# Kernel tuning notes

Measured on AMD Instinct MI355X. Metric: run time of the kernel, lower is better.

## Reference

```python
import jax, jax.numpy as jnp
import numpy as np

M, N, T = 32, 32, 512
H1 = (M + N) * 10 * 8      # 5120
H2 = M * N * 4             # 4096
HID = 1000                 # GRU hidden (hardcoded in module)
EPS = 1e-12


def _l2norm(x):
    # torch.nn.functional.normalize: x / max(||x||_2, eps)
    return x / jnp.maximum(jnp.linalg.norm(x), EPS)


def setup_inputs() -> dict:
    key = jax.random.key(0)
    ks = jax.random.split(key, 16)
    rn = lambda k, shp, s: (jax.random.normal(k, shp, dtype=jnp.float32) * s)
    inp = {
        "y": rn(ks[0], (T, N), 1.0),
        "F": rn(ks[1], (M, M), 0.5 / np.sqrt(M)),   # stable dynamics
        "H": rn(ks[2], (N, M), 1.0 / np.sqrt(M)),
        "m1x0": rn(ks[3], (M,), 1.0),
        "h0": rn(ks[4], (HID,), 1.0),
        "W1": rn(ks[5], (H1, M + N), 1.0 / np.sqrt(M + N)),
        "b1": rn(ks[6], (H1,), 0.01),
        "Wih": rn(ks[7], (3 * HID, H1), 1.0 / np.sqrt(H1)),
        "bih": rn(ks[8], (3 * HID,), 0.01),
        "Whh": rn(ks[9], (3 * HID, HID), 1.0 / np.sqrt(HID)),
        "bhh": rn(ks[10], (3 * HID,), 0.01),
        "W2": rn(ks[11], (H2, HID), 1.0 / np.sqrt(HID)),
        "b2": rn(ks[12], (H2,), 0.01),
        "W3": rn(ks[13], (M * N, H2), 1.0 / np.sqrt(H2)),
        "b3": rn(ks[14], (M * N,), 0.01),
    }
    return inp


def reference(y, F, H, m1x0, h0, W1, b1, Wih, bih, Whh, bhh, W2, b2, W3, b3):
    m, n = F.shape[0], H.shape[0]

    def step(carry, yt):
        m1x_prior, m1x_post, h = carry
        # step_prior
        m1x_prev_prior = m1x_prior
        m1x_prior = F @ m1x_post              # [m]
        m1y = H @ m1x_prior                   # [n]
        # step_KGain_est: features
        dm1x_n = _l2norm(m1x_post - m1x_prev_prior)
        dm1y_n = _l2norm(yt - m1y)
        kin = jnp.concatenate([dm1y_n, dm1x_n])  # [n+m]
        # KGain_step: Linear+ReLU -> single-step GRU -> Linear+ReLU -> Linear
        x = jax.nn.relu(W1 @ kin + b1)        # [H1]
        gi = Wih @ x + bih                    # [3*HID]
        gh = Whh @ h + bhh
        ir, iz, ic = jnp.split(gi, 3)
        hr, hz, hc = jnp.split(gh, 3)
        r = jax.nn.sigmoid(ir + hr)
        z = jax.nn.sigmoid(iz + hz)
        c = jnp.tanh(ic + r * hc)
        h_new = (1.0 - z) * c + z * h         # GRU hidden [HID]
        l2 = jax.nn.relu(W2 @ h_new + b2)     # [H2]
        KG = (W3 @ l2 + b3).reshape(m, n)     # Kalman gain
        # KNet_step: innovation update
        m1x_post_new = m1x_prior + KG @ (yt - m1y)
        return (m1x_prior, m1x_post_new, h_new), m1x_post_new

    init = (m1x0, m1x0, h0)
    _, posts = jax.lax.scan(step, init, y)
    return posts  # [T, m]
```

## Files before the change

kernel.cpp:

```cpp
#include <hip/hip_runtime.h>
#include <cmath>

#define Mdim 32
#define Ndim 32
#define Tsteps 512
#define H1dim 5120
#define H2dim 4096
#define HIDdim 1000
#define NWG 256
#define NTHR 1024

typedef unsigned int u32;
typedef unsigned short u16;

__device__ u16 g_w2b[H2dim * HIDdim];
__device__ u16 g_w3t[H2dim * Mdim * Ndim];

#define OFF_WIH 0
#define OFF_WHH 122880
#define OFF_UNION 146880
#define OFF_H9 157120
#define OFF_MISC 161640
#define SMEM_BYTES 162560

#define MI_POST 0
#define MI_PRIOR 32
#define MI_PREV 64
#define MI_INNOV 96
#define MI_KIN 128
#define MI_GI 192
#define MI_GH 204

__device__ __forceinline__ u16 f2bf(float f) {
  u32 u = __float_as_uint(f);
  return (u16)((u + 0x7fffu + ((u >> 16) & 1u)) >> 16);
}
__device__ __forceinline__ float bflo(u32 u) { return __uint_as_float(u << 16); }
__device__ __forceinline__ float bfhi(u32 u) { return __uint_as_float(u & 0xffff0000u); }

__device__ __forceinline__ float dot4(float4 a, float4 b) {
  return a.x * b.x + a.y * b.y + a.z * b.z + a.w * b.w;
}
__device__ __forceinline__ float dot8_bb(uint4 a, uint4 b) {
  float s = 0.f;
  s = fmaf(bflo(a.x), bflo(b.x), s); s = fmaf(bfhi(a.x), bfhi(b.x), s);
  s = fmaf(bflo(a.y), bflo(b.y), s); s = fmaf(bfhi(a.y), bfhi(b.y), s);
  s = fmaf(bflo(a.z), bflo(b.z), s); s = fmaf(bfhi(a.z), bfhi(b.z), s);
  s = fmaf(bflo(a.w), bflo(b.w), s); s = fmaf(bfhi(a.w), bfhi(b.w), s);
  return s;
}
__device__ __forceinline__ float dot8_bf(uint4 a, const float* x8) {
  float s = 0.f;
  s = fmaf(bflo(a.x), x8[0], s); s = fmaf(bfhi(a.x), x8[1], s);
  s = fmaf(bflo(a.y), x8[2], s); s = fmaf(bfhi(a.y), x8[3], s);
  s = fmaf(bflo(a.z), x8[4], s); s = fmaf(bfhi(a.z), x8[5], s);
  s = fmaf(bflo(a.w), x8[6], s); s = fmaf(bfhi(a.w), x8[7], s);
  return s;
}

__device__ __forceinline__ float wave_reduce64(float v) {
#pragma unroll
  for (int off = 32; off >= 1; off >>= 1) v += __shfl_xor(v, off, 64);
  return v;
}
__device__ __forceinline__ float group16_reduce(float v) {
#pragma unroll
  for (int off = 8; off >= 1; off >>= 1) v += __shfl_xor(v, off, 64);
  return v;
}

__device__ __forceinline__ float4 ldg_cg4(const float* p) {
  float4 r;
  asm volatile("global_load_dwordx4 %0, %1, off sc0 sc1\n\ts_waitcnt vmcnt(0)"
               : "=v"(r) : "v"(p) : "memory");
  return r;
}
__device__ __forceinline__ uint4 ldg_cg4u(const void* p) {
  uint4 r;
  asm volatile("global_load_dwordx4 %0, %1, off sc0 sc1\n\ts_waitcnt vmcnt(0)"
               : "=v"(r) : "v"(p) : "memory");
  return r;
}
__device__ __forceinline__ void ldg2_cg4(const float* p0, const float* p1,
                                         float4& r0, float4& r1) {
  asm volatile("global_load_dwordx4 %0, %2, off sc0 sc1\n\t"
               "global_load_dwordx4 %1, %3, off sc0 sc1\n\t"
               "s_waitcnt vmcnt(0)"
               : "=&v"(r0), "=&v"(r1) : "v"(p0), "v"(p1) : "memory");
}
__device__ __forceinline__ void stg_cg1(float* p, float v) {
  asm volatile("global_store_dword %0, %1, off sc0 sc1" :: "v"(p), "v"(v) : "memory");
}
__device__ __forceinline__ void stg_cg_u16(u16* p, u16 v) {
  u32 vv = v;
  asm volatile("global_store_short %0, %1, off sc0 sc1" :: "v"(p), "v"(vv) : "memory");
}

__device__ __forceinline__ void gridbar(u32* bar, u32 nb) {
  asm volatile("s_waitcnt vmcnt(0)" ::: "memory");
  __syncthreads();
  if (threadIdx.x == 0) {
    u32 g = (u32)blockIdx.x & 15u;
    u32 a = __hip_atomic_fetch_add(bar + g * 16, 1u, __ATOMIC_RELAXED,
                                   __HIP_MEMORY_SCOPE_AGENT);
    if ((a & 15u) == 15u) {
      u32 b = __hip_atomic_fetch_add(bar + 256, 1u, __ATOMIC_RELAXED,
                                     __HIP_MEMORY_SCOPE_AGENT);
      if ((b & 15u) == 15u)
        __hip_atomic_fetch_add(bar + 320, 1u, __ATOMIC_RELAXED,
                               __HIP_MEMORY_SCOPE_AGENT);
    }
    while (__hip_atomic_load(bar + 320, __ATOMIC_RELAXED,
                             __HIP_MEMORY_SCOPE_AGENT) < nb)
      __builtin_amdgcn_s_sleep(2);
  }
  __syncthreads();
}

__global__ void convert_w2(const float* __restrict__ W2) {
  int i = blockIdx.x * 1024 + threadIdx.x;
  if (i < H2dim * HIDdim) g_w2b[i] = f2bf(W2[i]);
}

__global__ void convert_w3t(const float* __restrict__ W3) {
  __shared__ float tile[32][33];
  int tr = blockIdx.x >> 7;
  int tc = blockIdx.x & 127;
  int r0 = tr * 32, c0 = tc * 32;
  int j = threadIdx.x & 31, i0 = threadIdx.x >> 5;
#pragma unroll
  for (int p = 0; p < 4; ++p) {
    int i = i0 + p * 8;
    tile[i][j] = W3[(size_t)(r0 + i) * H2dim + c0 + j];
  }
  __syncthreads();
#pragma unroll
  for (int p = 0; p < 4; ++p) {
    int i = i0 + p * 8;
    g_w3t[(size_t)(c0 + i) * 1024 + r0 + j] = f2bf(tile[j][i]);
  }
}

__global__ void __launch_bounds__(NTHR)
knet_kernel(const float* __restrict__ y, const float* __restrict__ F,
            const float* __restrict__ Hm, const float* __restrict__ m1x0,
            const float* __restrict__ h0, const float* __restrict__ W1,
            const float* __restrict__ b1, const float* __restrict__ Wih,
            const float* __restrict__ bih, const float* __restrict__ Whh,
            const float* __restrict__ bhh, const float* __restrict__ b2,
            const float* __restrict__ b3, float* __restrict__ out,
            u32* bar, u16* xb, float* hbuf, float* dpart) {
  extern __shared__ char smem[];
  u16* s_wih = (u16*)(smem + OFF_WIH);
  u16* s_whh = (u16*)(smem + OFF_WHH);
  u16* s_x = (u16*)(smem + OFF_UNION);
  float4* s_red4 = (float4*)(smem + OFF_UNION);
  float* s_redf = (float*)(smem + OFF_UNION);
  float* s_pd = (float*)(smem + OFF_UNION);
  float* s_h9 = (float*)(smem + OFF_H9);
  float* s_m = (float*)(smem + OFF_MISC);
  float* s_post = s_m + MI_POST;
  float* s_prior = s_m + MI_PRIOR;
  float* s_prev = s_m + MI_PREV;
  float* s_innov = s_m + MI_INNOV;
  float* s_kin = s_m + MI_KIN;
  float* s_gi = s_m + MI_GI;
  float* s_gh = s_m + MI_GH;

  const int tid = threadIdx.x;
  const int w = tid >> 6;
  const int lane = tid & 63;
  const int wg = blockIdx.x;
  const int k0 = wg * 4;
  const bool gru_wg = (wg < 250);
  u32 nb = 0;

  if (gru_wg) {
#pragma unroll 1
    for (int r = 0; r < 12; ++r) {
      const float* src = Wih + (size_t)((r >> 2) * HIDdim + k0 + (r & 3)) * H1dim;
      u16* dst = s_wih + r * H1dim;
      for (int e = tid; e < H1dim; e += NTHR) dst[e] = f2bf(src[e]);
    }
#pragma unroll 1
    for (int r = 0; r < 12; ++r) {
      const float* src = Whh + (size_t)((r >> 2) * HIDdim + k0 + (r & 3)) * HIDdim;
      u16* dst = s_whh + r * HIDdim;
      for (int e = tid; e < HIDdim; e += NTHR) dst[e] = f2bf(src[e]);
    }
  }
  if (tid < 250) {
    float4 hv = ((const float4*)h0)[tid];
    int b0 = tid * 4;
    s_h9[((b0 + 0) >> 3) * 9 + ((b0 + 0) & 7)] = hv.x;
    s_h9[((b0 + 1) >> 3) * 9 + ((b0 + 1) & 7)] = hv.y;
    s_h9[((b0 + 2) >> 3) * 9 + ((b0 + 2) & 7)] = hv.z;
    s_h9[((b0 + 3) >> 3) * 9 + ((b0 + 3) & 7)] = hv.w;
  }
  if (tid < Mdim) s_prior[tid] = m1x0[tid];
  __syncthreads();

  for (int t = 0; t < Tsteps; ++t) {
    if (t > 0) {
      float4 a0, a1;
      ldg2_cg4(dpart + tid * 4, dpart + (tid + 1024) * 4, a0, a1);
      float4 s;
      s.x = a0.x + a1.x; s.y = a0.y + a1.y; s.z = a0.z + a1.z; s.w = a0.w + a1.w;
#pragma unroll
      for (int off = 8; off <= 32; off <<= 1) {
        s.x += __shfl_xor(s.x, off, 64);
        s.y += __shfl_xor(s.y, off, 64);
        s.z += __shfl_xor(s.z, off, 64);
        s.w += __shfl_xor(s.w, off, 64);
      }
      if (lane < 8) s_red4[w * 8 + lane] = s;
    }
    __syncthreads();
    if (tid < Mdim) {
      float p;
      if (t == 0) {
        p = m1x0[tid];
      } else {
        float d = 0.f;
#pragma unroll
        for (int ww = 0; ww < 16; ++ww) d += s_redf[ww * 32 + tid];
        float bb = 0.f;
#pragma unroll 8
        for (int j = 0; j < 32; ++j) bb = fmaf(b3[tid * 32 + j], s_innov[j], bb);
        p = s_prior[tid] + d + bb;
        if (wg == 0) out[(t - 1) * Mdim + tid] = p;
      }
      s_prev[tid] = s_prior[tid];
      s_post[tid] = p;
    }
    __syncthreads();
    if (tid < Mdim) {
      float s = 0.f;
      const float4* Fr = (const float4*)(F + tid * Mdim);
      const float4* pp = (const float4*)s_post;
#pragma unroll
      for (int j = 0; j < 8; ++j) s += dot4(Fr[j], pp[j]);
      s_prior[tid] = s;
    }
    __syncthreads();
    if (tid < Ndim) {
      float s = 0.f;
      const float4* Hr = (const float4*)(Hm + tid * Mdim);
      const float4* pp = (const float4*)s_prior;
#pragma unroll
      for (int j = 0; j < 8; ++j) s += dot4(Hr[j], pp[j]);
      s_innov[tid] = y[t * Ndim + tid] - s;
    }
    __syncthreads();
    if (tid < 64) {
      float v = (tid < Ndim) ? s_innov[tid] : (s_post[tid - Ndim] - s_prev[tid - Ndim]);
      float sq = v * v;
#pragma unroll
      for (int off = 16; off >= 1; off >>= 1) sq += __shfl_xor(sq, off, 32);
      s_kin[tid] = v / fmaxf(sqrtf(sq), 1e-12f);
    }
    __syncthreads();
    if (w < 5) {
      int g = lane >> 4, k = lane & 15;
      int row = wg * 20 + w * 4 + g;
      float s = dot4(((const float4*)W1)[row * 16 + k], ((const float4*)s_kin)[k]);
      s = group16_reduce(s);
      if (k == 0) stg_cg_u16(xb + row, f2bf(fmaxf(s + b1[row], 0.f)));
    } else if (gru_wg && w >= 12) {
      int base = (w - 12) * 3;
#pragma unroll
      for (int rr = 0; rr < 3; ++rr) {
        int r = base + rr;
        const uint4* wr = (const uint4*)(s_whh + r * HIDdim);
        float acc = dot8_bf(wr[lane], s_h9 + lane * 9);
        if (lane < 61) acc += dot8_bf(wr[lane + 64], s_h9 + (lane + 64) * 9);
        acc = wave_reduce64(acc);
        if (lane == 0) s_gh[r] = acc + bhh[(r >> 2) * HIDdim + k0 + (r & 3)];
      }
    }
    gridbar(bar, ++nb);

    if (gru_wg) {
      if (tid < 640) ((uint4*)s_x)[tid] = ldg_cg4u((const char*)xb + tid * 16);
      __syncthreads();
      if (w < 12) {
        const uint4* wr = (const uint4*)(s_wih + w * H1dim);
        const uint4* xr = (const uint4*)s_x;
        float acc = 0.f;
#pragma unroll
        for (int i = 0; i < 10; ++i) {
          int j = lane + 64 * i;
          acc += dot8_bb(wr[j], xr[j]);
        }
        acc = wave_reduce64(acc);
        if (lane == 0) s_gi[w] = acc + bih[(w >> 2) * HIDdim + k0 + (w & 3)];
      }
      __syncthreads();
      if (tid < 4) {
        int k = k0 + tid;
        float hold = s_h9[(k >> 3) * 9 + (k & 7)];
        float ir = s_gi[tid], iz = s_gi[4 + tid], ic = s_gi[8 + tid];
        float r = 1.f / (1.f + expf(-(ir + s_gh[tid])));
        float z = 1.f / (1.f + expf(-(iz + s_gh[4 + tid])));
        float c_ = tanhf(ic + r * s_gh[8 + tid]);
        stg_cg1(hbuf + k, (1.f - z) * c_ + z * hold);
      }
    }
    gridbar(bar, ++nb);

    if (tid < 250) {
      float4 hv = ldg_cg4(hbuf + tid * 4);
      int b0 = tid * 4;
      s_h9[((b0 + 0) >> 3) * 9 + ((b0 + 0) & 7)] = hv.x;
      s_h9[((b0 + 1) >> 3) * 9 + ((b0 + 1) & 7)] = hv.y;
      s_h9[((b0 + 2) >> 3) * 9 + ((b0 + 2) & 7)] = hv.z;
      s_h9[((b0 + 3) >> 3) * 9 + ((b0 + 3) & 7)] = hv.w;
    }
    __syncthreads();
    {
      int c = wg * 16 + w;
      const uint4* wr = (const uint4*)(g_w2b + (size_t)c * HIDdim);
      float acc = dot8_bf(wr[lane], s_h9 + lane * 9);
      if (lane < 61) acc += dot8_bf(wr[lane + 64], s_h9 + (lane + 64) * 9);
      acc = wave_reduce64(acc);
      float l2c = fmaxf(acc + b2[c], 0.f);
      const uint4* tr3 = (const uint4*)(g_w3t + (size_t)c * 1024);
      uint4 t0 = tr3[2 * lane], t1 = tr3[2 * lane + 1];
      const float* iv = s_innov + 16 * (lane & 1);
      float u = dot8_bf(t0, iv) + dot8_bf(t1, iv + 8);
      u += __shfl_xor(u, 1, 64);
      if ((lane & 1) == 0) s_pd[w * 32 + (lane >> 1)] = l2c * u;
    }
    __syncthreads();
    if (tid < 32) {
      float pdv = 0.f;
#pragma unroll
      for (int ww = 0; ww < 16; ++ww) pdv += s_pd[ww * 32 + tid];
      stg_cg1(dpart + wg * 32 + tid, pdv);
    }
    gridbar(bar, ++nb);
  }

  if (wg == 0) {
    float4 a0, a1;
    ldg2_cg4(dpart + tid * 4, dpart + (tid + 1024) * 4, a0, a1);
    float4 s;
    s.x = a0.x + a1.x; s.y = a0.y + a1.y; s.z = a0.z + a1.z; s.w = a0.w + a1.w;
#pragma unroll
    for (int off = 8; off <= 32; off <<= 1) {
      s.x += __shfl_xor(s.x, off, 64);
      s.y += __shfl_xor(s.y, off, 64);
      s.z += __shfl_xor(s.z, off, 64);
      s.w += __shfl_xor(s.w, off, 64);
    }
    if (lane < 8) s_red4[w * 8 + lane] = s;
    __syncthreads();
    if (tid < Mdim) {
      float d = 0.f;
#pragma unroll
      for (int ww = 0; ww < 16; ++ww) d += s_redf[ww * 32 + tid];
      float bb = 0.f;
#pragma unroll 8
      for (int j = 0; j < 32; ++j) bb = fmaf(b3[tid * 32 + j], s_innov[j], bb);
      out[(Tsteps - 1) * Mdim + tid] = s_prior[tid] + d + bb;
    }
  }
}

extern "C" void kernel_launch(void* const* d_in, const int* in_sizes, int n_in,
                              void* d_out, int out_size, void* d_ws, size_t ws_size,
                              hipStream_t stream) {
  const float* y    = (const float*)d_in[0];
  const float* F    = (const float*)d_in[1];
  const float* Hm   = (const float*)d_in[2];
  const float* m1x0 = (const float*)d_in[3];
  const float* h0   = (const float*)d_in[4];
  const float* W1   = (const float*)d_in[5];
  const float* b1   = (const float*)d_in[6];
  const float* Wih  = (const float*)d_in[7];
  const float* bih  = (const float*)d_in[8];
  const float* Whh  = (const float*)d_in[9];
  const float* bhh  = (const float*)d_in[10];
  const float* W2   = (const float*)d_in[11];
  const float* b2   = (const float*)d_in[12];
  const float* W3   = (const float*)d_in[13];
  const float* b3   = (const float*)d_in[14];
  float* out = (float*)d_out;

  u32* bar   = (u32*)d_ws;
  u16* xb    = (u16*)((char*)d_ws + 4096);
  float* hbuf  = (float*)((char*)d_ws + 14336);
  float* dpart = (float*)((char*)d_ws + 18432);

  convert_w2<<<4000, 1024, 0, stream>>>(W2);
  convert_w3t<<<4096, 256, 0, stream>>>(W3);
  hipMemsetAsync(d_ws, 0, 4096, stream);
  hipFuncSetAttribute((const void*)knet_kernel,
                      hipFuncAttributeMaxDynamicSharedMemorySize, SMEM_BYTES);
  void* args[] = {&y, &F, &Hm, &m1x0, &h0, &W1, &b1, &Wih, &bih, &Whh, &bhh,
                  &b2, &b3, &out, &bar, &xb, &hbuf, &dpart};
  hipLaunchCooperativeKernel((const void*)knet_kernel, dim3(NWG), dim3(NTHR),
                             args, SMEM_BYTES, stream);
}
```

Measured before the change: 7.523 ms.

## Split grid barrier into arrive/wait and overlap independent work in the gaps

Replaces the hierarchical atomic grid barrier with a single-counter barrier split into arrive and wait phases. Work that does not depend on the barrier is moved between arrive and wait: the Whh·h product for the next step, the W3^T·innovation dot, the b3 term and the next y load. Per-block W2, W3, W1 and b2 weights are hoisted into registers once before the time loop. The small Kalman prior/innovation chain now runs inside one wave without block syncs. The aim is to shorten the serial per-step critical path dominated by grid barriers, but all 256 blocks now contend on a single atomic counter and register pressure rises.

```diff
diff --git a/kernel.cpp b/kernel.cpp
--- a/kernel.cpp
+++ b/kernel.cpp
@@ -9,6 +9,7 @@
 #define HIDdim 1000
 #define NWG 256
 #define NTHR 1024
+#define POLLER 320
 
 typedef unsigned int u32;
 typedef unsigned short u16;
@@ -25,7 +26,6 @@
 
 #define MI_POST 0
 #define MI_PRIOR 32
-#define MI_PREV 64
 #define MI_INNOV 96
 #define MI_KIN 128
 #define MI_GI 192
@@ -96,23 +96,16 @@
   asm volatile("global_store_short %0, %1, off sc0 sc1" :: "v"(p), "v"(vv) : "memory");
 }
 
-__device__ __forceinline__ void gridbar(u32* bar, u32 nb) {
+__device__ __forceinline__ void gb_arrive(u32* bar) {
   asm volatile("s_waitcnt vmcnt(0)" ::: "memory");
   __syncthreads();
-  if (threadIdx.x == 0) {
-    u32 g = (u32)blockIdx.x & 15u;
-    u32 a = __hip_atomic_fetch_add(bar + g * 16, 1u, __ATOMIC_RELAXED,
-                                   __HIP_MEMORY_SCOPE_AGENT);
-    if ((a & 15u) == 15u) {
-      u32 b = __hip_atomic_fetch_add(bar + 256, 1u, __ATOMIC_RELAXED,
-                                     __HIP_MEMORY_SCOPE_AGENT);
-      if ((b & 15u) == 15u)
-        __hip_atomic_fetch_add(bar + 320, 1u, __ATOMIC_RELAXED,
-                               __HIP_MEMORY_SCOPE_AGENT);
-    }
-    while (__hip_atomic_load(bar + 320, __ATOMIC_RELAXED,
-                             __HIP_MEMORY_SCOPE_AGENT) < nb)
-      __builtin_amdgcn_s_sleep(2);
+  if (threadIdx.x == POLLER)
+    __hip_atomic_fetch_add(bar, 1u, __ATOMIC_RELAXED, __HIP_MEMORY_SCOPE_AGENT);
+}
+__device__ __forceinline__ void gb_wait(u32* bar, u32 target) {
+  if (threadIdx.x == POLLER) {
+    while (__hip_atomic_load(bar, __ATOMIC_RELAXED, __HIP_MEMORY_SCOPE_AGENT) < target)
+      __builtin_amdgcn_s_sleep(1);
   }
   __syncthreads();
 }
@@ -161,7 +154,6 @@
   float* s_m = (float*)(smem + OFF_MISC);
   float* s_post = s_m + MI_POST;
   float* s_prior = s_m + MI_PRIOR;
-  float* s_prev = s_m + MI_PREV;
   float* s_innov = s_m + MI_INNOV;
   float* s_kin = s_m + MI_KIN;
   float* s_gi = s_m + MI_GI;
@@ -197,8 +189,44 @@
     s_h9[((b0 + 2) >> 3) * 9 + ((b0 + 2) & 7)] = hv.z;
     s_h9[((b0 + 3) >> 3) * 9 + ((b0 + 3) & 7)] = hv.w;
   }
-  if (tid < Mdim) s_prior[tid] = m1x0[tid];
   __syncthreads();
+
+  const int c2 = wg * 16 + w;
+  const uint4* w2p = (const uint4*)(g_w2b + (size_t)c2 * HIDdim);
+  uint4 wr0r = w2p[lane];
+  uint4 wr1r = make_uint4(0u, 0u, 0u, 0u);
+  if (lane < 61) wr1r = w2p[lane + 64];
+  const uint4* w3p = (const uint4*)(g_w3t + (size_t)c2 * 1024);
+  uint4 t0r = w3p[2 * lane];
+  uint4 t1r = w3p[2 * lane + 1];
+  const float b2c = b2[c2];
+  float4 w1c = make_float4(0.f, 0.f, 0.f, 0.f);
+  float b1c = 0.f;
+  int w1row = 0;
+  if (w < 5) {
+    w1row = wg * 20 + w * 4 + (lane >> 4);
+    w1c = ((const float4*)W1)[w1row * 16 + (lane & 15)];
+    b1c = b1[w1row];
+  }
+  float prior = 0.f, bb = 0.f, yv = 0.f;
+  if (w == 0 && lane < 32) {
+    prior = m1x0[lane];
+    yv = y[lane];
+  }
+
+  auto gh_compute = [&]() {
+    int base = (w - 12) * 3;
+#pragma unroll
+    for (int rr = 0; rr < 3; ++rr) {
+      int r = base + rr;
+      const uint4* wr = (const uint4*)(s_whh + r * HIDdim);
+      float acc = dot8_bf(wr[lane], s_h9 + lane * 9);
+      if (lane < 61) acc += dot8_bf(wr[lane + 64], s_h9 + (lane + 64) * 9);
+      acc = wave_reduce64(acc);
+      if (lane == 0) s_gh[r] = acc + bhh[(r >> 2) * HIDdim + k0 + (r & 3)];
+    }
+  };
+  if (gru_wg && w >= 12) gh_compute();
 
   for (int t = 0; t < Tsteps; ++t) {
     if (t > 0) {
@@ -216,69 +244,57 @@
       if (lane < 8) s_red4[w * 8 + lane] = s;
     }
     __syncthreads();
-    if (tid < Mdim) {
-      float p;
-      if (t == 0) {
-        p = m1x0[tid];
-      } else {
-        float d = 0.f;
-#pragma unroll
-        for (int ww = 0; ww < 16; ++ww) d += s_redf[ww * 32 + tid];
-        float bb = 0.f;
-#pragma unroll 8
-        for (int j = 0; j < 32; ++j) bb = fmaf(b3[tid * 32 + j], s_innov[j], bb);
-        p = s_prior[tid] + d + bb;
-        if (wg == 0) out[(t - 1) * Mdim + tid] = p;
-      }
-      s_prev[tid] = s_prior[tid];
-      s_post[tid] = p;
-    }
-    __syncthreads();
-    if (tid < Mdim) {
-      float s = 0.f;
-      const float4* Fr = (const float4*)(F + tid * Mdim);
-      const float4* pp = (const float4*)s_post;
-#pragma unroll
-      for (int j = 0; j < 8; ++j) s += dot4(Fr[j], pp[j]);
-      s_prior[tid] = s;
-    }
-    __syncthreads();
-    if (tid < Ndim) {
-      float s = 0.f;
-      const float4* Hr = (const float4*)(Hm + tid * Mdim);
-      const float4* pp = (const float4*)s_prior;
-#pragma unroll
-      for (int j = 0; j < 8; ++j) s += dot4(Hr[j], pp[j]);
-      s_innov[tid] = y[t * Ndim + tid] - s;
-    }
-    __syncthreads();
-    if (tid < 64) {
-      float v = (tid < Ndim) ? s_innov[tid] : (s_post[tid - Ndim] - s_prev[tid - Ndim]);
+    if (w == 0) {
+      float p = 0.f, inn = 0.f;
+      float prev = prior;
+      if (lane < 32) {
+        if (t == 0) {
+          p = m1x0[lane];
+        } else {
+          float dsum = 0.f;
+#pragma unroll
+          for (int ww = 0; ww < 16; ++ww) dsum += s_redf[ww * 32 + lane];
+          p = prior + dsum + bb;
+          if (wg == 0) out[(t - 1) * Mdim + lane] = p;
+        }
+        s_post[lane] = p;
+      }
+      asm volatile("" ::: "memory");
+      if (lane < 32) {
+        const float4* Fr = (const float4*)(F + lane * Mdim);
+        const float4* pp = (const float4*)s_post;
+        float s = 0.f;
+#pragma unroll
+        for (int j = 0; j < 8; ++j) s += dot4(Fr[j], pp[j]);
+        prior = s;
+        s_prior[lane] = s;
+      }
+      asm volatile("" ::: "memory");
+      if (lane < 32) {
+        const float4* Hr = (const float4*)(Hm + lane * Mdim);
+        const float4* pp = (const float4*)s_prior;
+        float s = 0.f;
+#pragma unroll
+        for (int j = 0; j < 8; ++j) s += dot4(Hr[j], pp[j]);
+        inn = yv - s;
+        s_innov[lane] = inn;
+      }
+      float vd = __shfl(p, lane & 31, 64) - __shfl(prev, lane & 31, 64);
+      float v = (lane < 32) ? inn : vd;
       float sq = v * v;
 #pragma unroll
       for (int off = 16; off >= 1; off >>= 1) sq += __shfl_xor(sq, off, 32);
-      s_kin[tid] = v / fmaxf(sqrtf(sq), 1e-12f);
+      s_kin[lane] = v / fmaxf(sqrtf(sq), 1e-12f);
     }
     __syncthreads();
     if (w < 5) {
-      int g = lane >> 4, k = lane & 15;
-      int row = wg * 20 + w * 4 + g;
-      float s = dot4(((const float4*)W1)[row * 16 + k], ((const float4*)s_kin)[k]);
+      float s = dot4(w1c, ((const float4*)s_kin)[lane & 15]);
       s = group16_reduce(s);
-      if (k == 0) stg_cg_u16(xb + row, f2bf(fmaxf(s + b1[row], 0.f)));
-    } else if (gru_wg && w >= 12) {
-      int base = (w - 12) * 3;
-#pragma unroll
-      for (int rr = 0; rr < 3; ++rr) {
-        int r = base + rr;
-        const uint4* wr = (const uint4*)(s_whh + r * HIDdim);
-        float acc = dot8_bf(wr[lane], s_h9 + lane * 9);
-        if (lane < 61) acc += dot8_bf(wr[lane + 64], s_h9 + (lane + 64) * 9);
-        acc = wave_reduce64(acc);
-        if (lane == 0) s_gh[r] = acc + bhh[(r >> 2) * HIDdim + k0 + (r & 3)];
-      }
-    }
-    gridbar(bar, ++nb);
+      if ((lane & 15) == 0) stg_cg_u16(xb + w1row, f2bf(fmaxf(s + b1c, 0.f)));
+    }
+    ++nb;
+    gb_arrive(bar);
+    gb_wait(bar, nb * NWG);
 
     if (gru_wg) {
       if (tid < 640) ((uint4*)s_x)[tid] = ldg_cg4u((const char*)xb + tid * 16);
@@ -306,7 +322,15 @@
         stg_cg1(hbuf + k, (1.f - z) * c_ + z * hold);
       }
     }
-    gridbar(bar, ++nb);
+    ++nb;
+    gb_arrive(bar);
+    float u;
+    {
+      const float* iv = s_innov + 16 * (lane & 1);
+      u = dot8_bf(t0r, iv) + dot8_bf(t1r, iv + 8);
+      u += __shfl_xor(u, 1, 64);
+    }
+    gb_wait(bar, nb * NWG);
 
     if (tid < 250) {
       float4 hv = ldg_cg4(hbuf + tid * 4);
@@ -318,17 +342,10 @@
     }
     __syncthreads();
     {
-      int c = wg * 16 + w;
-      const uint4* wr = (const uint4*)(g_w2b + (size_t)c * HIDdim);
-      float acc = dot8_bf(wr[lane], s_h9 + lane * 9);
-      if (lane < 61) acc += dot8_bf(wr[lane + 64], s_h9 + (lane + 64) * 9);
+      float acc = dot8_bf(wr0r, s_h9 + lane * 9);
+      if (lane < 61) acc += dot8_bf(wr1r, s_h9 + (lane + 64) * 9);
       acc = wave_reduce64(acc);
-      float l2c = fmaxf(acc + b2[c], 0.f);
-      const uint4* tr3 = (const uint4*)(g_w3t + (size_t)c * 1024);
-      uint4 t0 = tr3[2 * lane], t1 = tr3[2 * lane + 1];
-      const float* iv = s_innov + 16 * (lane & 1);
-      float u = dot8_bf(t0, iv) + dot8_bf(t1, iv + 8);
-      u += __shfl_xor(u, 1, 64);
+      float l2c = fmaxf(acc + b2c, 0.f);
       if ((lane & 1) == 0) s_pd[w * 32 + (lane >> 1)] = l2c * u;
     }
     __syncthreads();
@@ -338,7 +355,18 @@
       for (int ww = 0; ww < 16; ++ww) pdv += s_pd[ww * 32 + tid];
       stg_cg1(dpart + wg * 32 + tid, pdv);
     }
-    gridbar(bar, ++nb);
+    ++nb;
+    gb_arrive(bar);
+    if (gru_wg && w >= 12) gh_compute();
+    if (w == 0 && lane < 32) {
+      int tn = (t + 1 < Tsteps) ? t + 1 : Tsteps - 1;
+      yv = y[tn * Ndim + lane];
+      float b = 0.f;
+#pragma unroll 8
+      for (int j = 0; j < 32; ++j) b = fmaf(b3[lane * 32 + j], s_innov[j], b);
+      bb = b;
+    }
+    gb_wait(bar, nb * NWG);
   }
 
   if (wg == 0) {
@@ -355,14 +383,11 @@
     }
     if (lane < 8) s_red4[w * 8 + lane] = s;
     __syncthreads();
-    if (tid < Mdim) {
+    if (w == 0 && lane < 32) {
       float d = 0.f;
 #pragma unroll
-      for (int ww = 0; ww < 16; ++ww) d += s_redf[ww * 32 + tid];
-      float bb = 0.f;
-#pragma unroll 8
-      for (int j = 0; j < 32; ++j) bb = fmaf(b3[tid * 32 + j], s_innov[j], bb);
-      out[(Tsteps - 1) * Mdim + tid] = s_prior[tid] + d + bb;
+      for (int ww = 0; ww < 16; ++ww) d += s_redf[ww * 32 + lane];
+      out[(Tsteps - 1) * Mdim + lane] = prior + d + bb;
     }
   }
 }
```

After: 11.87 ms. +57.7%, slower.
